# Kernel tuning notes

Hardware: AMD Instinct MI355X
Metric: run time of the kernel (lower is better)

## Reference

```python
import jax, jax.numpy as jnp
import numpy as np

B, Q, P = 8, 300, 5
RS, QS, CS, NC = 256, 768, 768, 396
HW = [64, 32, 16, 8]
POOL = [32, 16, 8, 4]
THR = 0.2


def _ln(x, g, b, eps=1e-5):
    m = x.mean(-1, keepdims=True)
    v = ((x - m) ** 2).mean(-1, keepdims=True)
    return (x - m) / jnp.sqrt(v + eps) * g + b


def _avgpool(x, oh, ow):
    # exact adaptive avg pool (output divides input)
    b, c, h, w = x.shape
    return x.reshape(b, c, oh, h // oh, ow, w // ow).mean((3, 5))


def setup_inputs() -> dict:
    key = jax.random.key(0)
    ks = jax.random.split(key, 40)
    inp = {}
    inp['pred_logits'] = jax.random.normal(ks[0], (B, Q, P), dtype=jnp.float32)
    inp['pred_boxes'] = jax.random.uniform(ks[1], (B, Q, 4), dtype=jnp.float32)
    inp['hs'] = jax.random.normal(ks[2], (B, Q, RS), dtype=jnp.float32)
    for s in range(4):
        inp[f'feat{s}'] = jax.random.normal(ks[3 + s], (B, 256, HW[s], HW[s]), dtype=jnp.float32)
        inp[f'pos{s}'] = jax.random.normal(ks[7 + s], (B, 256, HW[s], HW[s]), dtype=jnp.float32)
        inp[f'mask{s}'] = jax.random.bernoulli(ks[11 + s], 0.15, (B, HW[s], HW[s]))
        inp[f'convW{s}'] = jax.random.normal(ks[15 + s], (CS, 256), dtype=jnp.float32) * 0.02
        inp[f'convb{s}'] = jnp.zeros((CS,), jnp.float32)
        inp[f'lng{s}'] = jnp.ones((CS,), jnp.float32)
        inp[f'lnb{s}'] = jnp.zeros((CS,), jnp.float32)
    inp['learnable_query'] = jax.random.normal(ks[19], (P + 1, QS), dtype=jnp.float32)
    inp['Wq'] = jax.random.normal(ks[20], (RS, QS), dtype=jnp.float32) * 0.02
    inp['bq'] = jnp.zeros((QS,), jnp.float32)
    inp['qng'] = jnp.ones((QS,), jnp.float32)
    inp['qnb'] = jnp.zeros((QS,), jnp.float32)
    inp['W1'] = jax.random.normal(ks[21], (QS, QS), dtype=jnp.float32) * 0.02
    inp['b1'] = jnp.zeros((QS,), jnp.float32)
    inp['W2'] = jax.random.normal(ks[22], (QS, NC), dtype=jnp.float32) * 0.02
    inp['b2'] = jnp.zeros((NC,), jnp.float32)
    return inp


def _forward(pred_logits, pred_boxes, hs,
             feats, poss, masks, convWs, convbs, lngs, lnbs,
             learnable_query, Wq, bq, qng, qnb, W1, b1, W2, b2):
    del pred_boxes  # selected in the original but never used
    b = hs.shape[0]
    prob = jax.nn.sigmoid(pred_logits)                       # (B,Q,P)
    # per-prompt membership: logit_i > thr (implies max > thr)
    m = (prob > THR).astype(hs.dtype)                        # (B,Q,P)
    cnt = m.sum(1)                                           # (B,P)
    ssum = jnp.einsum('bqp,bqd->bpd', m, hs)                 # segment-sum over queries
    pooled = jnp.where(cnt[..., None] > 0,
                       ssum / jnp.maximum(cnt, 1.0)[..., None], 0.0)  # (B,P,RS)
    proj = pooled @ Wq + bq                                  # (B,P,QS)
    any_sel = jnp.any(prob.max(-1) > THR, axis=1)            # (B,)
    # if no query passed the global gate, prompt_hs is zeros WITHOUT projection
    prompt_hs = jnp.where(any_sel[:, None, None], proj, 0.0)
    prompt_query = learnable_query[1:] + prompt_hs           # (B,P,QS)
    cls_query = jnp.broadcast_to(learnable_query[0][None, None, :], (b, 1, QS))
    query_tokens = jnp.concatenate([cls_query, prompt_query], axis=1)
    query_tokens = _ln(query_tokens, qng, qnb)               # (B,P+1,QS)

    tokens = []
    for s in range(4):
        mask_f = masks[s][:, None, :, :].astype(feats[s].dtype)   # (B,1,H,W)
        x = (feats[s] + poss[s]) * (1.0 - mask_f)                 # masked_fill
        ctx = jnp.einsum('bchw,oc->bohw', x, convWs[s]) + convbs[s][None, :, None, None]
        p = _avgpool(ctx, POOL[s], POOL[s])
        mp = jnp.clip(_avgpool(1.0 - mask_f, POOL[s], POOL[s]), 1e-6, None)
        p = p / mp
        t = p.reshape(b, CS, -1).transpose(0, 2, 1)               # (B,T_s,CS)
        tokens.append(_ln(t, lngs[s], lnbs[s]))
    ctx_all = jnp.concatenate(tokens, axis=1)                     # (B,1360,CS)

    # encoder stand-in: fuse context into query tokens additively
    last = query_tokens + ctx_all.mean(1)[:, None, :]
    cls_logit = last[:, 0]
    prompt_logit = last[:, 1:].mean(1)
    h = jax.nn.relu((cls_logit + prompt_logit) @ W1 + b1)
    return h @ W2 + b2                                            # (B,NC)


def reference(pred_logits, pred_boxes, hs,
              feat0, pos0, mask0, convW0, convb0, lng0, lnb0,
              feat1, pos1, mask1, convW1, convb1, lng1, lnb1,
              feat2, pos2, mask2, convW2, convb2, lng2, lnb2,
              feat3, pos3, mask3, convW3, convb3, lng3, lnb3,
              learnable_query, Wq, bq, qng, qnb, W1, b1, W2, b2):
    return _forward(pred_logits, pred_boxes, hs,
                    [feat0, feat1, feat2, feat3],
                    [pos0, pos1, pos2, pos3],
                    [mask0, mask1, mask2, mask3],
                    [convW0, convW1, convW2, convW3],
                    [convb0, convb1, convb2, convb3],
                    [lng0, lng1, lng2, lng3],
                    [lnb0, lnb1, lnb2, lnb3],
                    learnable_query, Wq, bq, qng, qnb, W1, b1, W2, b2)
```

## Files before the change

### kernel.cpp

```cpp
#include <hip/hip_runtime.h>
#include <hip/hip_bf16.h>

#define Bn 8
#define Qn 300
#define Pn 5
#define RSn 256
#define QSn 768
#define NCn 396
#define MTOT 10880
#define THRL -1.3862943611198906f

typedef __attribute__((ext_vector_type(8))) short short8;
typedef __attribute__((ext_vector_type(4))) float float4v;

__device__ inline float wred(float v){
  #pragma unroll
  for (int off = 32; off; off >>= 1) v += __shfl_xor(v, off);
  return v;
}

__device__ __forceinline__ unsigned short f2bf(float f){
  union { float f; unsigned int u; } c; c.f = f;
  return (unsigned short)((c.u + 0x7FFF + ((c.u >> 16) & 1)) >> 16);
}

__device__ __forceinline__ void gld_lds16(const short* g, short* l){
  __builtin_amdgcn_global_load_lds(
      (const __attribute__((address_space(1))) void*)g,
      (__attribute__((address_space(3))) void*)l, 16, 0, 0);
}

__device__ __forceinline__ void mask_w(const void* M, int mbase, int mode, int i00, int H,
                                       float* w){
  if (mode == 0){
    int4 ma = *(const int4*)((const int*)M + mbase + i00);
    int4 mb = *(const int4*)((const int*)M + mbase + i00 + H);
    w[0]=ma.x?0.f:1.f; w[1]=ma.y?0.f:1.f; w[2]=ma.z?0.f:1.f; w[3]=ma.w?0.f:1.f;
    w[4]=mb.x?0.f:1.f; w[5]=mb.y?0.f:1.f; w[6]=mb.z?0.f:1.f; w[7]=mb.w?0.f:1.f;
  } else if (mode == 1){
    const unsigned char* Mb = (const unsigned char*)M + mbase;
    uchar4 ma = *(const uchar4*)(Mb + i00);
    uchar4 mb = *(const uchar4*)(Mb + i00 + H);
    w[0]=ma.x?0.f:1.f; w[1]=ma.y?0.f:1.f; w[2]=ma.z?0.f:1.f; w[3]=ma.w?0.f:1.f;
    w[4]=mb.x?0.f:1.f; w[5]=mb.y?0.f:1.f; w[6]=mb.z?0.f:1.f; w[7]=mb.w?0.f:1.f;
  } else {
    float4 ma = *(const float4*)((const float*)M + mbase + i00);
    float4 mb = *(const float4*)((const float*)M + mbase + i00 + H);
    w[0]=1.f-ma.x; w[1]=1.f-ma.y; w[2]=1.f-ma.z; w[3]=1.f-ma.w;
    w[4]=1.f-mb.x; w[5]=1.f-mb.y; w[6]=1.f-mb.z; w[7]=1.f-mb.w;
  }
}

__global__ __launch_bounds__(256, 4) void k_front(
    const float* cw0, const float* cw1, const float* cw2, const float* cw3,
    short* Wswz, const int* __restrict__ m0, int* det,
    const float* __restrict__ pl, const float* __restrict__ hs,
    float* pooled, int* flags, float* ctxsum, float* outz){
  int bx = blockIdx.x;
  int t = threadIdx.x;
  if (bx < 768){
    int s = bx / 192;
    int linear = (bx % 192)*256 + t;
    int q = linear & 63, n = linear >> 6;
    const float* src = (s==0)?cw0:(s==1)?cw1:(s==2)?cw2:cw3;
    float4 f = *(const float4*)(src + (size_t)n*256 + q*4);
    int kc = q >> 3, lk = (q >> 1) & 3, e0 = (q & 1)*4;
    short* dst = Wswz + ((size_t)(s*8 + kc))*24576 + lk*6144 + n*8 + e0;
    short4 sv;
    sv.x = (short)f2bf(f.x); sv.y = (short)f2bf(f.y);
    sv.z = (short)f2bf(f.z); sv.w = (short)f2bf(f.w);
    *(short4*)dst = sv;
    return;
  }
  if (bx == 768){
    __shared__ int r0[4], r1[4];
    const int* mm = m0 + t*32;
    int d0 = 0, d1 = 0;
    #pragma unroll 8
    for (int i = 0; i < 32; ++i){
      int v = mm[i];
      d0 |= (v != 0 && v != 1);
      d1 |= (v != 0 && v != 0x3F800000);
    }
    unsigned long long bal0 = __ballot(d0), bal1 = __ballot(d1);
    int wid = t >> 6;
    if ((t & 63) == 0){ r0[wid] = (bal0 != 0ull); r1[wid] = (bal1 != 0ull); }
    __syncthreads();
    if (t == 0){
      det[0] = r0[0] | r0[1] | r0[2] | r0[3];
      det[1] = r1[0] | r1[1] | r1[2] | r1[3];
    }
    return;
  }
  if (bx >= 821){
    int idx = ((bx - 821)*256 + t)*4;
    if (idx < Bn*NCn) *(float4*)(outz + idx) = (float4){0.f,0.f,0.f,0.f};
    return;
  }
  if (bx >= 809){
    int idx = ((bx - 809)*256 + t)*4;
    *(float4*)(ctxsum + idx) = (float4){0.f,0.f,0.f,0.f};
    return;
  }
  __shared__ float msk[Qn];
  int bb = (bx - 769) / Pn, p = (bx - 769) % Pn;
  for (int q = t; q < Qn; q += 256)
    msk[q] = (pl[(bb*Qn + q)*Pn + p] > THRL) ? 1.f : 0.f;
  __syncthreads();
  const float* hb = hs + (size_t)bb*Qn*RSn + t;
  float s0 = 0.f, s1 = 0.f, s2 = 0.f, s3 = 0.f, cnt = 0.f;
  for (int q = 0; q < Qn; q += 4){
    float m0v = msk[q], m1 = msk[q+1], m2 = msk[q+2], m3 = msk[q+3];
    cnt += m0v + m1 + m2 + m3;
    s0 = fmaf(m0v, hb[(size_t)(q  )*RSn], s0);
    s1 = fmaf(m1,  hb[(size_t)(q+1)*RSn], s1);
    s2 = fmaf(m2,  hb[(size_t)(q+2)*RSn], s2);
    s3 = fmaf(m3,  hb[(size_t)(q+3)*RSn], s3);
  }
  float ssum = (s0 + s1) + (s2 + s3);
  pooled[(bb*Pn + p)*RSn + t] = (cnt > 0.f) ? ssum / cnt : 0.f;
  if (t == 0) flags[bb*Pn + p] = (cnt > 0.f) ? 1 : 0;
}

__global__ __launch_bounds__(256, 4) void k_mid(
    const float* f0, const float* p0, const void* m0,
    const float* f1, const float* p1, const void* m1,
    const float* f2, const float* p2, const void* m2,
    const float* f3, const float* p3, const void* m3,
    const int* __restrict__ det, unsigned short* ATb, float* invmp,
    const float* __restrict__ lq, const float* __restrict__ Wq,
    const float* __restrict__ bq, const float* __restrict__ qng,
    const float* __restrict__ qnb, const float* __restrict__ pooled,
    const int* __restrict__ flags, float* qt){
  __shared__ float pq[256];
  __shared__ float s1s[4], s2s[4];
  int bx = blockIdx.x;
  int t = threadIdx.x;
  if (bx >= 48){
    int p = bx - 48;
    int mode = (det[0] == 0) ? 0 : ((det[1] == 0) ? 2 : 1);
    if (p < 1024){
      int b = p >> 7, r = p & 127;
      int c0 = (r >> 1)*4, half = r & 1;
      const int H = 64, HH = 4096;
      int tk = half*256 + t;
      int ph = tk >> 4, pw = tk & 15;
      int i00 = ph*128 + pw*4;
      int mbase = b*HH;
      float w[8];
      mask_w(m0, mbase, mode, i00, H, w);
      size_t plane = (size_t)(b*256 + c0)*HH + i00;
      const float* Fb = f0 + plane;
      const float* Pb = p0 + plane;
      float4 FA0 = *(const float4*)(Fb);
      float4 FB0 = *(const float4*)(Fb + H);
      float4 PA0 = *(const float4*)(Pb);
      float4 PB0 = *(const float4*)(Pb + H);
      float4 FA1 = *(const float4*)(Fb + HH);
      float4 FB1 = *(const float4*)(Fb + HH + H);
      float4 PA1 = *(const float4*)(Pb + HH);
      float4 PB1 = *(const float4*)(Pb + HH + H);
      float4 FA2 = *(const float4*)(Fb + 2*HH);
      float4 FB2 = *(const float4*)(Fb + 2*HH + H);
      float4 PA2 = *(const float4*)(Pb + 2*HH);
      float4 PB2 = *(const float4*)(Pb + 2*HH + H);
      float4 FA3 = *(const float4*)(Fb + 3*HH);
      float4 FB3 = *(const float4*)(Fb + 3*HH + H);
      float4 PA3 = *(const float4*)(Pb + 3*HH);
      float4 PB3 = *(const float4*)(Pb + 3*HH + H);
      float ms0 = w[0]+w[1]+w[4]+w[5];
      float ms1 = w[2]+w[3]+w[6]+w[7];
      float im0 = 1.f / fmaxf(ms0*0.25f, 1e-6f);
      float im1 = 1.f / fmaxf(ms1*0.25f, 1e-6f);
      float sc0 = 0.25f*im0, sc1 = 0.25f*im1;
      int mIdx = b*1024 + tk*2;
      #define DO_CH(cc, FA, FB, PA, PB) { \
        float x0 = (FA.x+PA.x)*w[0] + (FA.y+PA.y)*w[1] + (FB.x+PB.x)*w[4] + (FB.y+PB.y)*w[5]; \
        float x1 = (FA.z+PA.z)*w[2] + (FA.w+PA.w)*w[3] + (FB.z+PB.z)*w[6] + (FB.w+PB.w)*w[7]; \
        *(unsigned int*)(ATb + (size_t)(c0+cc)*MTOT + mIdx) = \
            (unsigned int)f2bf(x0*sc0) | ((unsigned int)f2bf(x1*sc1) << 16); }
      DO_CH(0, FA0, FB0, PA0, PB0)
      DO_CH(1, FA1, FB1, PA1, PB1)
      DO_CH(2, FA2, FB2, PA2, PB2)
      DO_CH(3, FA3, FB3, PA3, PB3)
      #undef DO_CH
      if (c0 == 0){ invmp[mIdx] = im0; invmp[mIdx+1] = im1; }
      return;
    }
    const float* F; const float* Pp; const void* M; int H, SB, T;
    int b, ch, tk; bool wr;
    if (p < 1536){
      int idx = p - 1024; b = idx >> 6;
      int c0 = (idx & 63)*4;
      F=f1; Pp=p1; M=m1; H=32; SB=8192; T=256;
      int ci = t >> 7; tk = t & 127;
      ch = c0 + ci*2; wr = (ch == 0);
      int ph = tk >> 3, pw = tk & 7;
      int i00 = ph*64 + pw*4;
      int HH = H*H, mbase = b*HH;
      float w[8]; mask_w(M, mbase, mode, i00, H, w);
      float ms0 = w[0]+w[1]+w[4]+w[5];
      float ms1 = w[2]+w[3]+w[6]+w[7];
      float im0 = 1.f / fmaxf(ms0*0.25f, 1e-6f);
      float im1 = 1.f / fmaxf(ms1*0.25f, 1e-6f);
      float sc0 = 0.25f*im0, sc1 = 0.25f*im1;
      int mIdx = SB + b*T + tk*2;
      size_t plane = (size_t)(b*256 + ch)*HH + i00;
      const float* Fb = F + plane; const float* Pb = Pp + plane;
      float4 FA0 = *(const float4*)(Fb);
      float4 FB0 = *(const float4*)(Fb + H);
      float4 PA0 = *(const float4*)(Pb);
      float4 PB0 = *(const float4*)(Pb + H);
      float4 FA1 = *(const float4*)(Fb + HH);
      float4 FB1 = *(const float4*)(Fb + HH + H);
      float4 PA1 = *(const float4*)(Pb + HH);
      float4 PB1 = *(const float4*)(Pb + HH + H);
      {
        float x0 = (FA0.x+PA0.x)*w[0] + (FA0.y+PA0.y)*w[1] + (FB0.x+PB0.x)*w[4] + (FB0.y+PB0.y)*w[5];
        float x1 = (FA0.z+PA0.z)*w[2] + (FA0.w+PA0.w)*w[3] + (FB0.z+PB0.z)*w[6] + (FB0.w+PB0.w)*w[7];
        *(unsigned int*)(ATb + (size_t)ch*MTOT + mIdx) =
            (unsigned int)f2bf(x0*sc0) | ((unsigned int)f2bf(x1*sc1) << 16);
        float y0 = (FA1.x+PA1.x)*w[0] + (FA1.y+PA1.y)*w[1] + (FB1.x+PB1.x)*w[4] + (FB1.y+PB1.y)*w[5];
        float y1 = (FA1.z+PA1.z)*w[2] + (FA1.w+PA1.w)*w[3] + (FB1.z+PB1.z)*w[6] + (FB1.w+PB1.w)*w[7];
        *(unsigned int*)(ATb + (size_t)(ch+1)*MTOT + mIdx) =
            (unsigned int)f2bf(y0*sc0) | ((unsigned int)f2bf(y1*sc1) << 16);
      }
      if (wr){ invmp[mIdx] = im0; invmp[mIdx+1] = im1; }
      return;
    }
    if (p < 1792){
      int idx = p - 1536; b = idx >> 5;
      ch = ((idx & 31)*8) + (t >> 5); tk = t & 31;
      F=f2; Pp=p2; M=m2; H=16; SB=10240; T=64;
    } else {
      int idx = p - 1792; b = idx >> 3;
      ch = ((idx & 7)*32) + (t >> 3); tk = t & 7;
      F=f3; Pp=p3; M=m3; H=8; SB=10752; T=16;
    }
    wr = (ch == 0);
    int OW2 = H >> 2;
    int ph = tk / OW2, pw = tk - ph*OW2;
    int i00 = ph*2*H + pw*4;
    int HH = H*H, mbase = b*HH;
    float w[8]; mask_w(M, mbase, mode, i00, H, w);
    float ms0 = w[0]+w[1]+w[4]+w[5];
    float ms1 = w[2]+w[3]+w[6]+w[7];
    float im0 = 1.f / fmaxf(ms0*0.25f, 1e-6f);
    float im1 = 1.f / fmaxf(ms1*0.25f, 1e-6f);
    float sc0 = 0.25f*im0, sc1 = 0.25f*im1;
    int mIdx = SB + b*T + tk*2;
    size_t plane = (size_t)(b*256 + ch)*HH + i00;
    const float* Fb = F + plane; const float* Pb = Pp + plane;
    float4 FA = *(const float4*)(Fb);
    float4 FB = *(const float4*)(Fb + H);
    float4 PA = *(const float4*)(Pb);
    float4 PB = *(const float4*)(Pb + H);
    float x0 = (FA.x+PA.x)*w[0] + (FA.y+PA.y)*w[1] + (FB.x+PB.x)*w[4] + (FB.y+PB.y)*w[5];
    float x1 = (FA.z+PA.z)*w[2] + (FA.w+PA.w)*w[3] + (FB.z+PB.z)*w[6] + (FB.w+PB.w)*w[7];
    *(unsigned int*)(ATb + (size_t)ch*MTOT + mIdx) =
        (unsigned int)f2bf(x0*sc0) | ((unsigned int)f2bf(x1*sc1) << 16);
    if (wr){ invmp[mIdx] = im0; invmp[mIdx+1] = im1; }
    return;
  }
  int b = bx / 6, j = bx % 6;
  float v0 = lq[j*QSn + t], v1 = lq[j*QSn + t + 256], v2 = lq[j*QSn + t + 512];
  int any = flags[b*Pn] | flags[b*Pn+1] | flags[b*Pn+2] | flags[b*Pn+3] | flags[b*Pn+4];
  if (j > 0 && any){
    pq[t] = pooled[(b*Pn + (j-1))*RSn + t];
    __syncthreads();
    float a0 = 0.f, a1 = 0.f, a2 = 0.f;
    #pragma unroll 8
    for (int c = 0; c < RSn; ++c){
      float pv = pq[c];
      a0 = fmaf(pv, Wq[c*QSn + t      ], a0);
      a1 = fmaf(pv, Wq[c*QSn + t + 256], a1);
      a2 = fmaf(pv, Wq[c*QSn + t + 512], a2);
    }
    v0 += a0 + bq[t]; v1 += a1 + bq[t+256]; v2 += a2 + bq[t+512];
  }
  float sm = v0 + v1 + v2, sq = v0*v0 + v1*v1 + v2*v2;
  sm = wred(sm); sq = wred(sq);
  int wid = t >> 6, lane = t & 63;
  if (lane == 0){ s1s[wid] = sm; s2s[wid] = sq; }
  __syncthreads();
  float S  = s1s[0] + s1s[1] + s1s[2] + s1s[3];
  float SQ = s2s[0] + s2s[1] + s2s[2] + s2s[3];
  float mu = S * (1.f/QSn), var = SQ * (1.f/QSn) - mu*mu;
  float rs = rsqrtf(var + 1e-5f);
  float* o = qt + (b*6 + j)*QSn;
  o[t      ] = (v0 - mu)*rs*qng[t      ] + qnb[t      ];
  o[t + 256] = (v1 - mu)*rs*qng[t + 256] + qnb[t + 256];
  o[t + 512] = (v2 - mu)*rs*qng[t + 512] + qnb[t + 512];
}

__global__ __launch_bounds__(256, 2) void k_gemm_ln(
    const unsigned short* __restrict__ ATb, const short* __restrict__ Wswz,
    const float* __restrict__ invmp,
    const float* cb0, const float* cb1, const float* cb2, const float* cb3,
    const float* lg0, const float* lb0, const float* lg1, const float* lb1,
    const float* lg2, const float* lb2, const float* lg3, const float* lb3,
    float* __restrict__ ctxsum){
  __shared__ short Bsh[24576];
  __shared__ float lsum[4][32], lsq[4][32];
  int m0 = blockIdx.x * 32;
  int s;
  if (m0 < 8192) s = 0;
  else if (m0 < 10240) s = 1;
  else if (m0 < 10752) s = 2;
  else s = 3;
  int b0, b1;
  if (s == 0){ b0 = m0 >> 10; b1 = b0; }
  else if (s == 1){ b0 = (m0 - 8192) >> 8; b1 = b0; }
  else if (s == 2){ b0 = (m0 - 10240) >> 6; b1 = b0; }
  else { b0 = (m0 - 10752) >> 4; b1 = b0 + 1; }
  const float *CB, *LG, *LB;
  if (s==0){ CB=cb0; LG=lg0; LB=lb0; }
  else if (s==1){ CB=cb1; LG=lg1; LB=lb1; }
  else if (s==2){ CB=cb2; LG=lg2; LB=lb2; }
  else { CB=cb3; LG=lg3; LB=lb3; }

  int t = threadIdx.x;
  int wid = t >> 6, l = t & 63;
  int lm = l & 15, lk = l >> 4;
  int nfb = wid * 12;

  {
    const unsigned short* src = ATb + (size_t)t*MTOT + m0;
    short8 a0 = *(const short8*)(src);
    short8 a1 = *(const short8*)(src + 8);
    short8 a2 = *(const short8*)(src + 16);
    short8 a3 = *(const short8*)(src + 24);
    #pragma unroll
    for (int e = 0; e < 8; ++e){
      Bsh[e*264 + t]      = a0[e];
      Bsh[(e+8)*264 + t]  = a1[e];
      Bsh[(e+16)*264 + t] = a2[e];
      Bsh[(e+24)*264 + t] = a3[e];
    }
  }
  __syncthreads();
  short8 aReg[2][8];
  #pragma unroll
  for (int mt = 0; mt < 2; ++mt)
    #pragma unroll
    for (int kc = 0; kc < 8; ++kc)
      aReg[mt][kc] = *(const short8*)(Bsh + (mt*16 + lm)*264 + kc*32 + lk*8);
  __syncthreads();

  float4v acc[2][12];
  #pragma unroll
  for (int mt = 0; mt < 2; ++mt)
    #pragma unroll
    for (int nf = 0; nf < 12; ++nf) acc[mt][nf] = (float4v){0.f,0.f,0.f,0.f};

  #pragma unroll
  for (int kc = 0; kc < 8; ++kc){
    const short* slice = Wswz + ((size_t)(s*8 + kc))*24576;
    #pragma unroll
    for (int j = 0; j < 12; ++j){
      int chunk = wid*12 + j;
      gld_lds16(slice + chunk*512 + l*8, Bsh + chunk*512);
    }
    __syncthreads();
    const short* bb = Bsh + lk*6144 + lm*8;
    #pragma unroll
    for (int nf = 0; nf < 12; ++nf){
      short8 bf = *(const short8*)(bb + (size_t)(nfb+nf)*128);
      acc[0][nf] = __builtin_amdgcn_mfma_f32_16x16x32_bf16(aReg[0][kc], bf, acc[0][nf], 0, 0, 0);
      acc[1][nf] = __builtin_amdgcn_mfma_f32_16x16x32_bf16(aReg[1][kc], bf, acc[1][nf], 0, 0, 0);
    }
    __syncthreads();
  }

  float im[2][4];
  #pragma unroll
  for (int mt = 0; mt < 2; ++mt)
    #pragma unroll
    for (int r = 0; r < 4; ++r) im[mt][r] = invmp[m0 + mt*16 + lk*4 + r];

  float sum[2][4] = {{0,0,0,0},{0,0,0,0}}, sq[2][4] = {{0,0,0,0},{0,0,0,0}};
  #pragma unroll
  for (int nf = 0; nf < 12; ++nf){
    float cbv = CB[(nfb+nf)*16 + lm];
    #pragma unroll
    for (int mt = 0; mt < 2; ++mt)
      #pragma unroll
      for (int r = 0; r < 4; ++r){
        float p = acc[mt][nf][r] + cbv*im[mt][r];
        acc[mt][nf][r] = p;
        sum[mt][r] += p;
        sq[mt][r] = fmaf(p, p, sq[mt][r]);
      }
  }
  #pragma unroll
  for (int mt = 0; mt < 2; ++mt)
    #pragma unroll
    for (int r = 0; r < 4; ++r){
      #pragma unroll
      for (int off = 1; off < 16; off <<= 1){
        sum[mt][r] += __shfl_xor(sum[mt][r], off);
        sq[mt][r]  += __shfl_xor(sq[mt][r],  off);
      }
    }
  if (lm == 0){
    #pragma unroll
    for (int mt = 0; mt < 2; ++mt)
      #pragma unroll
      for (int r = 0; r < 4; ++r){
        lsum[wid][mt*16 + lk*4 + r] = sum[mt][r];
        lsq[wid][mt*16 + lk*4 + r]  = sq[mt][r];
      }
  }
  __syncthreads();
  float mu[2][4], rs[2][4];
  #pragma unroll
  for (int mt = 0; mt < 2; ++mt)
    #pragma unroll
    for (int r = 0; r < 4; ++r){
      int row = mt*16 + lk*4 + r;
      float S  = lsum[0][row] + lsum[1][row] + lsum[2][row] + lsum[3][row];
      float SQ = lsq[0][row]  + lsq[1][row]  + lsq[2][row]  + lsq[3][row];
      mu[mt][r] = S * (1.f/768.f);
      float var = SQ * (1.f/768.f) - mu[mt][r]*mu[mt][r];
      rs[mt][r] = rsqrtf(var + 1e-5f);
    }
  #pragma unroll
  for (int nf = 0; nf < 12; ++nf){
    int n = (nfb+nf)*16 + lm;
    float g = LG[n], bb2 = LB[n];
    float tv0 = 0.f, tv1 = 0.f;
    #pragma unroll
    for (int r = 0; r < 4; ++r){
      tv0 += (acc[0][nf][r] - mu[0][r]) * rs[0][r];
      tv1 += (acc[1][nf][r] - mu[1][r]) * rs[1][r];
    }
    tv0 = tv0*g + 4.f*bb2;
    tv1 = tv1*g + 4.f*bb2;
    tv0 += __shfl_xor(tv0, 16); tv0 += __shfl_xor(tv0, 32);
    tv1 += __shfl_xor(tv1, 16); tv1 += __shfl_xor(tv1, 32);
    if (lk == 0){
      atomicAdd(&ctxsum[b0*768 + n], tv0);
      atomicAdd(&ctxsum[b1*768 + n], tv1);
    }
  }
}

__global__ void k_hpre(const float* __restrict__ qt, const float* __restrict__ ctxsum,
                       const float* __restrict__ W1, const float* __restrict__ b1,
                       float* __restrict__ hpre){
  __shared__ float vsh[Bn][192];
  int nc = blockIdx.x % 24, kc = blockIdx.x / 24;
  int n0 = nc*32, c0 = kc*192;
  int t = threadIdx.x;
  for (int i = t; i < Bn*192; i += 256){
    int b = i / 192, cl = i - b*192;
    int c = c0 + cl;
    const float* q = qt + (size_t)b*6*768;
    float pm = q[768+c] + q[2*768+c] + q[3*768+c] + q[4*768+c] + q[5*768+c];
    vsh[b][cl] = q[c] + 0.2f*pm + ctxsum[b*768 + c]*(1.f/680.f);
  }
  __syncthreads();
  int ow = t & 31, bi = t >> 5;
  int o = n0 + ow;
  float acc = 0.f;
  const float* w = W1 + (size_t)c0*768 + o;
  #pragma unroll 4
  for (int cl = 0; cl < 192; ++cl)
    acc = fmaf(vsh[bi][cl], w[(size_t)cl*768], acc);
  if (kc == 0) acc += b1[o];
  atomicAdd(&hpre[bi*768 + o], acc);
}

__global__ void k_out(const float* __restrict__ hpre, const float* __restrict__ W2,
                      const float* __restrict__ b2, float* __restrict__ out){
  __shared__ float hsh[Bn][192];
  int nc = blockIdx.x % 13, kc = blockIdx.x / 13;
  int n0 = nc*32, c0 = kc*192;
  int t = threadIdx.x;
  for (int i = t; i < Bn*192; i += 256){
    int b = i / 192, cl = i - b*192;
    hsh[b][cl] = fmaxf(hpre[b*768 + c0 + cl], 0.f);
  }
  __syncthreads();
  int ow = t & 31, bi = t >> 5;
  int o = n0 + ow;
  if (o >= NCn) return;
  float acc = 0.f;
  const float* w = W2 + (size_t)c0*NCn + o;
  #pragma unroll 4
  for (int cl = 0; cl < 192; ++cl)
    acc = fmaf(hsh[bi][cl], w[(size_t)cl*NCn], acc);
  if (kc == 0) acc += b2[o];
  atomicAdd(&out[bi*NCn + o], acc);
}

extern "C" void kernel_launch(void* const* d_in, const int* in_sizes, int n_in,
                              void* d_out, int out_size, void* d_ws, size_t ws_size,
                              hipStream_t stream){
  const float* pl = (const float*)d_in[0];
  const float* hs = (const float*)d_in[2];
  const float* feat[4]; const float* pos[4]; const void* mask[4];
  const float* cw[4]; const float* cb[4]; const float* lg[4]; const float* lb[4];
  for (int s = 0; s < 4; ++s){
    int base = 3 + 7*s;
    feat[s] = (const float*)d_in[base];
    pos[s]  = (const float*)d_in[base+1];
    mask[s] = d_in[base+2];
    cw[s]   = (const float*)d_in[base+3];
    cb[s]   = (const float*)d_in[base+4];
    lg[s]   = (const float*)d_in[base+5];
    lb[s]   = (const float*)d_in[base+6];
  }
  const float* lq  = (const float*)d_in[31];
  const float* Wq  = (const float*)d_in[32];
  const float* bq  = (const float*)d_in[33];
  const float* qng = (const float*)d_in[34];
  const float* qnb = (const float*)d_in[35];
  const float* W1  = (const float*)d_in[36];
  const float* b1  = (const float*)d_in[37];
  const float* W2  = (const float*)d_in[38];
  const float* b2  = (const float*)d_in[39];
  float* out = (float*)d_out;

  unsigned short* ATb = (unsigned short*)d_ws;
  short* Wswz   = (short*)(ATb + (size_t)256*MTOT);
  float* invmp  = (float*)(Wswz + (size_t)4*8*4*768*8);
  float* pooled = invmp + MTOT;
  float* qt     = pooled + 40*RSn;
  float* ctxsum = qt + Bn*6*QSn;
  float* hpre   = ctxsum + Bn*QSn;
  int*   det    = (int*)(hpre + Bn*QSn);
  int*   flags  = det + 4;

  k_front<<<825, 256, 0, stream>>>(cw[0], cw[1], cw[2], cw[3], Wswz,
                                   (const int*)mask[0], det, pl, hs, pooled, flags,
                                   ctxsum, out);
  k_mid<<<1904, 256, 0, stream>>>(feat[0], pos[0], mask[0],
                                  feat[1], pos[1], mask[1],
                                  feat[2], pos[2], mask[2],
                                  feat[3], pos[3], mask[3],
                                  det, ATb, invmp,
                                  lq, Wq, bq, qng, qnb, pooled, flags, qt);
  k_gemm_ln<<<340, 256, 0, stream>>>(ATb, Wswz, invmp,
                                     cb[0], cb[1], cb[2], cb[3],
                                     lg[0], lb[0], lg[1], lb[1],
                                     lg[2], lb[2], lg[3], lb[3], ctxsum);
  k_hpre<<<96, 256, 0, stream>>>(qt, ctxsum, W1, b1, hpre);
  k_out<<<52, 256, 0, stream>>>(hpre, W2, b2, out);
}
```

Baseline: 285.6 us.

## Fuse masked pooling into GEMM+LayerNorm kernel, drop bf16 activation buffer

Merges the pooling kernel into the GEMM+LN kernel. Each 32-row tile now computes its masked average pool directly from feat+pos into shared memory, so the bf16 activation buffer and inverse-mask array no longer go through global memory. This removes one launch and the global round trip of the pooled activations. In exchange, each block issues narrower float2 loads with less parallelism in the gather, and the query-norm blocks now share the heavier kernel's shared-memory footprint and occupancy.

```diff
diff --git a/kernel.cpp b/kernel.cpp
--- a/kernel.cpp
+++ b/kernel.cpp
@@ -30,30 +30,9 @@
       (__attribute__((address_space(3))) void*)l, 16, 0, 0);
 }
 
-__device__ __forceinline__ void mask_w(const void* M, int mbase, int mode, int i00, int H,
-                                       float* w){
-  if (mode == 0){
-    int4 ma = *(const int4*)((const int*)M + mbase + i00);
-    int4 mb = *(const int4*)((const int*)M + mbase + i00 + H);
-    w[0]=ma.x?0.f:1.f; w[1]=ma.y?0.f:1.f; w[2]=ma.z?0.f:1.f; w[3]=ma.w?0.f:1.f;
-    w[4]=mb.x?0.f:1.f; w[5]=mb.y?0.f:1.f; w[6]=mb.z?0.f:1.f; w[7]=mb.w?0.f:1.f;
-  } else if (mode == 1){
-    const unsigned char* Mb = (const unsigned char*)M + mbase;
-    uchar4 ma = *(const uchar4*)(Mb + i00);
-    uchar4 mb = *(const uchar4*)(Mb + i00 + H);
-    w[0]=ma.x?0.f:1.f; w[1]=ma.y?0.f:1.f; w[2]=ma.z?0.f:1.f; w[3]=ma.w?0.f:1.f;
-    w[4]=mb.x?0.f:1.f; w[5]=mb.y?0.f:1.f; w[6]=mb.z?0.f:1.f; w[7]=mb.w?0.f:1.f;
-  } else {
-    float4 ma = *(const float4*)((const float*)M + mbase + i00);
-    float4 mb = *(const float4*)((const float*)M + mbase + i00 + H);
-    w[0]=1.f-ma.x; w[1]=1.f-ma.y; w[2]=1.f-ma.z; w[3]=1.f-ma.w;
-    w[4]=1.f-mb.x; w[5]=1.f-mb.y; w[6]=1.f-mb.z; w[7]=1.f-mb.w;
-  }
-}
-
 __global__ __launch_bounds__(256, 4) void k_front(
     const float* cw0, const float* cw1, const float* cw2, const float* cw3,
-    short* Wswz, const int* __restrict__ m0, int* det,
+    short* Wswz, const int* __restrict__ mk0, int* det,
     const float* __restrict__ pl, const float* __restrict__ hs,
     float* pooled, int* flags, float* ctxsum, float* outz){
   int bx = blockIdx.x;
@@ -74,7 +53,7 @@
   }
   if (bx == 768){
     __shared__ int r0[4], r1[4];
-    const int* mm = m0 + t*32;
+    const int* mm = mk0 + t*32;
     int d0 = 0, d1 = 0;
     #pragma unroll 8
     for (int i = 0; i < 32; ++i){
@@ -122,230 +101,150 @@
   if (t == 0) flags[bb*Pn + p] = (cnt > 0.f) ? 1 : 0;
 }
 
-__global__ __launch_bounds__(256, 4) void k_mid(
-    const float* f0, const float* p0, const void* m0,
-    const float* f1, const float* p1, const void* m1,
-    const float* f2, const float* p2, const void* m2,
-    const float* f3, const float* p3, const void* m3,
-    const int* __restrict__ det, unsigned short* ATb, float* invmp,
+__global__ __launch_bounds__(256, 2) void k_pgemm(
+    const float* fe0, const float* po0, const void* ma0,
+    const float* fe1, const float* po1, const void* ma1,
+    const float* fe2, const float* po2, const void* ma2,
+    const float* fe3, const float* po3, const void* ma3,
+    const int* __restrict__ det, const short* __restrict__ Wswz,
+    const float* cb0, const float* cb1, const float* cb2, const float* cb3,
+    const float* lg0, const float* lb0, const float* lg1, const float* lb1,
+    const float* lg2, const float* lb2, const float* lg3, const float* lb3,
+    float* __restrict__ ctxsum,
     const float* __restrict__ lq, const float* __restrict__ Wq,
     const float* __restrict__ bq, const float* __restrict__ qng,
     const float* __restrict__ qnb, const float* __restrict__ pooled,
     const int* __restrict__ flags, float* qt){
+  __shared__ short Bsh[24576];
+  __shared__ short As[32*264];
+  __shared__ float wls[32][4];
+  __shared__ float scls[32], imls[32];
+  __shared__ float lsum[4][32], lsq[4][32];
   __shared__ float pq[256];
   __shared__ float s1s[4], s2s[4];
-  int bx = blockIdx.x;
+  int blk = blockIdx.x;
   int t = threadIdx.x;
-  if (bx >= 48){
-    int p = bx - 48;
-    int mode = (det[0] == 0) ? 0 : ((det[1] == 0) ? 2 : 1);
-    if (p < 1024){
-      int b = p >> 7, r = p & 127;
-      int c0 = (r >> 1)*4, half = r & 1;
-      const int H = 64, HH = 4096;
-      int tk = half*256 + t;
-      int ph = tk >> 4, pw = tk & 15;
-      int i00 = ph*128 + pw*4;
-      int mbase = b*HH;
-      float w[8];
-      mask_w(m0, mbase, mode, i00, H, w);
-      size_t plane = (size_t)(b*256 + c0)*HH + i00;
-      const float* Fb = f0 + plane;
-      const float* Pb = p0 + plane;
-      float4 FA0 = *(const float4*)(Fb);
-      float4 FB0 = *(const float4*)(Fb + H);
-      float4 PA0 = *(const float4*)(Pb);
-      float4 PB0 = *(const float4*)(Pb + H);
-      float4 FA1 = *(const float4*)(Fb + HH);
-      float4 FB1 = *(const float4*)(Fb + HH + H);
-      float4 PA1 = *(const float4*)(Pb + HH);
-      float4 PB1 = *(const float4*)(Pb + HH + H);
-      float4 FA2 = *(const float4*)(Fb + 2*HH);
-      float4 FB2 = *(const float4*)(Fb + 2*HH + H);
-      float4 PA2 = *(const float4*)(Pb + 2*HH);
-      float4 PB2 = *(const float4*)(Pb + 2*HH + H);
-      float4 FA3 = *(const float4*)(Fb + 3*HH);
-      float4 FB3 = *(const float4*)(Fb + 3*HH + H);
-      float4 PA3 = *(const float4*)(Pb + 3*HH);
-      float4 PB3 = *(const float4*)(Pb + 3*HH + H);
-      float ms0 = w[0]+w[1]+w[4]+w[5];
-      float ms1 = w[2]+w[3]+w[6]+w[7];
-      float im0 = 1.f / fmaxf(ms0*0.25f, 1e-6f);
-      float im1 = 1.f / fmaxf(ms1*0.25f, 1e-6f);
-      float sc0 = 0.25f*im0, sc1 = 0.25f*im1;
-      int mIdx = b*1024 + tk*2;
-      #define DO_CH(cc, FA, FB, PA, PB) { \
-        float x0 = (FA.x+PA.x)*w[0] + (FA.y+PA.y)*w[1] + (FB.x+PB.x)*w[4] + (FB.y+PB.y)*w[5]; \
-        float x1 = (FA.z+PA.z)*w[2] + (FA.w+PA.w)*w[3] + (FB.z+PB.z)*w[6] + (FB.w+PB.w)*w[7]; \
-        *(unsigned int*)(ATb + (size_t)(c0+cc)*MTOT + mIdx) = \
-            (unsigned int)f2bf(x0*sc0) | ((unsigned int)f2bf(x1*sc1) << 16); }
-      DO_CH(0, FA0, FB0, PA0, PB0)
-      DO_CH(1, FA1, FB1, PA1, PB1)
-      DO_CH(2, FA2, FB2, PA2, PB2)
-      DO_CH(3, FA3, FB3, PA3, PB3)
-      #undef DO_CH
-      if (c0 == 0){ invmp[mIdx] = im0; invmp[mIdx+1] = im1; }
-      return;
-    }
-    const float* F; const float* Pp; const void* M; int H, SB, T;
-    int b, ch, tk; bool wr;
-    if (p < 1536){
-      int idx = p - 1024; b = idx >> 6;
-      int c0 = (idx & 63)*4;
-      F=f1; Pp=p1; M=m1; H=32; SB=8192; T=256;
-      int ci = t >> 7; tk = t & 127;
-      ch = c0 + ci*2; wr = (ch == 0);
-      int ph = tk >> 3, pw = tk & 7;
-      int i00 = ph*64 + pw*4;
-      int HH = H*H, mbase = b*HH;
-      float w[8]; mask_w(M, mbase, mode, i00, H, w);
-      float ms0 = w[0]+w[1]+w[4]+w[5];
-      float ms1 = w[2]+w[3]+w[6]+w[7];
-      float im0 = 1.f / fmaxf(ms0*0.25f, 1e-6f);
-      float im1 = 1.f / fmaxf(ms1*0.25f, 1e-6f);
-      float sc0 = 0.25f*im0, sc1 = 0.25f*im1;
-      int mIdx = SB + b*T + tk*2;
-      size_t plane = (size_t)(b*256 + ch)*HH + i00;
-      const float* Fb = F + plane; const float* Pb = Pp + plane;
-      float4 FA0 = *(const float4*)(Fb);
-      float4 FB0 = *(const float4*)(Fb + H);
-      float4 PA0 = *(const float4*)(Pb);
-      float4 PB0 = *(const float4*)(Pb + H);
-      float4 FA1 = *(const float4*)(Fb + HH);
-      float4 FB1 = *(const float4*)(Fb + HH + H);
-      float4 PA1 = *(const float4*)(Pb + HH);
-      float4 PB1 = *(const float4*)(Pb + HH + H);
-      {
-        float x0 = (FA0.x+PA0.x)*w[0] + (FA0.y+PA0.y)*w[1] + (FB0.x+PB0.x)*w[4] + (FB0.y+PB0.y)*w[5];
-        float x1 = (FA0.z+PA0.z)*w[2] + (FA0.w+PA0.w)*w[3] + (FB0.z+PB0.z)*w[6] + (FB0.w+PB0.w)*w[7];
-        *(unsigned int*)(ATb + (size_t)ch*MTOT + mIdx) =
-            (unsigned int)f2bf(x0*sc0) | ((unsigned int)f2bf(x1*sc1) << 16);
-        float y0 = (FA1.x+PA1.x)*w[0] + (FA1.y+PA1.y)*w[1] + (FB1.x+PB1.x)*w[4] + (FB1.y+PB1.y)*w[5];
-        float y1 = (FA1.z+PA1.z)*w[2] + (FA1.w+PA1.w)*w[3] + (FB1.z+PB1.z)*w[6] + (FB1.w+PB1.w)*w[7];
-        *(unsigned int*)(ATb + (size_t)(ch+1)*MTOT + mIdx) =
-            (unsigned int)f2bf(y0*sc0) | ((unsigned int)f2bf(y1*sc1) << 16);
+
+  if (blk >= 340){
+    int qbx = blk - 340;
+    int b = qbx / 6, j = qbx % 6;
+    float v0 = lq[j*QSn + t], v1 = lq[j*QSn + t + 256], v2 = lq[j*QSn + t + 512];
+    int any = flags[b*Pn] | flags[b*Pn+1] | flags[b*Pn+2] | flags[b*Pn+3] | flags[b*Pn+4];
+    if (j > 0 && any){
+      pq[t] = pooled[(b*Pn + (j-1))*RSn + t];
+      __syncthreads();
+      float a0 = 0.f, a1 = 0.f, a2 = 0.f;
+      #pragma unroll 8
+      for (int c = 0; c < RSn; ++c){
+        float pv = pq[c];
+        a0 = fmaf(pv, Wq[c*QSn + t      ], a0);
+        a1 = fmaf(pv, Wq[c*QSn + t + 256], a1);
+        a2 = fmaf(pv, Wq[c*QSn + t + 512], a2);
       }
-      if (wr){ invmp[mIdx] = im0; invmp[mIdx+1] = im1; }
-      return;
-    }
-    if (p < 1792){
-      int idx = p - 1536; b = idx >> 5;
-      ch = ((idx & 31)*8) + (t >> 5); tk = t & 31;
-      F=f2; Pp=p2; M=m2; H=16; SB=10240; T=64;
+      v0 += a0 + bq[t]; v1 += a1 + bq[t+256]; v2 += a2 + bq[t+512];
+    }
+    float sm = v0 + v1 + v2, sq = v0*v0 + v1*v1 + v2*v2;
+    sm = wred(sm); sq = wred(sq);
+    int wid = t >> 6, lane = t & 63;
+    if (lane == 0){ s1s[wid] = sm; s2s[wid] = sq; }
+    __syncthreads();
+    float S  = s1s[0] + s1s[1] + s1s[2] + s1s[3];
+    float SQ = s2s[0] + s2s[1] + s2s[2] + s2s[3];
+    float mu = S * (1.f/QSn), var = SQ * (1.f/QSn) - mu*mu;
+    float rs = rsqrtf(var + 1e-5f);
+    float* o = qt + (b*6 + j)*QSn;
+    o[t      ] = (v0 - mu)*rs*qng[t      ] + qnb[t      ];
+    o[t + 256] = (v1 - mu)*rs*qng[t + 256] + qnb[t + 256];
+    o[t + 512] = (v2 - mu)*rs*qng[t + 512] + qnb[t + 512];
+    return;
+  }
+
+  int m0 = blk * 32;
+  int s, H, OWlog, b0, b1;
+  const float *F, *Pp; const void* M;
+  const float *CB, *LG, *LB;
+  if (m0 < 8192){ s=0; F=fe0; Pp=po0; M=ma0; H=64; OWlog=5; b0=m0>>10; b1=b0;
+                  CB=cb0; LG=lg0; LB=lb0; }
+  else if (m0 < 10240){ s=1; F=fe1; Pp=po1; M=ma1; H=32; OWlog=4; b0=(m0-8192)>>8; b1=b0;
+                  CB=cb1; LG=lg1; LB=lb1; }
+  else if (m0 < 10752){ s=2; F=fe2; Pp=po2; M=ma2; H=16; OWlog=3; b0=(m0-10240)>>6; b1=b0;
+                  CB=cb2; LG=lg2; LB=lb2; }
+  else { s=3; F=fe3; Pp=po3; M=ma3; H=8; OWlog=2; b0=(m0-10752)>>4; b1=b0+1;
+                  CB=cb3; LG=lg3; LB=lb3; }
+  int HH = H*H;
+  int OWm = (H >> 1) - 1;
+  int mode = (det[0] == 0) ? 0 : ((det[1] == 0) ? 2 : 1);
+
+  int slot = t & 31;
+  int gm = m0 + slot;
+  int bb, ltl;
+  if (s == 0){ bb = gm >> 10; ltl = gm & 1023; }
+  else if (s == 1){ bb = (gm - 8192) >> 8; ltl = gm & 255; }
+  else if (s == 2){ bb = (gm - 10240) >> 6; ltl = gm & 63; }
+  else { bb = (gm - 10752) >> 4; ltl = gm & 15; }
+  int ph = ltl >> OWlog, pw = ltl & OWm;
+  int i00 = ph*2*H + pw*2;
+  int mbase = bb*HH;
+
+  if (t < 32){
+    float w0, w1, w2, w3;
+    if (mode == 0){
+      const int* Mi = (const int*)M + mbase + i00;
+      int2 ma = *(const int2*)(Mi);
+      int2 mb = *(const int2*)(Mi + H);
+      w0 = ma.x?0.f:1.f; w1 = ma.y?0.f:1.f; w2 = mb.x?0.f:1.f; w3 = mb.y?0.f:1.f;
+    } else if (mode == 1){
+      const unsigned char* Mb = (const unsigned char*)M + mbase + i00;
+      w0 = Mb[0]?0.f:1.f; w1 = Mb[1]?0.f:1.f; w2 = Mb[H]?0.f:1.f; w3 = Mb[H+1]?0.f:1.f;
     } else {
-      int idx = p - 1792; b = idx >> 3;
-      ch = ((idx & 7)*32) + (t >> 3); tk = t & 7;
-      F=f3; Pp=p3; M=m3; H=8; SB=10752; T=16;
-    }
-    wr = (ch == 0);
-    int OW2 = H >> 2;
-    int ph = tk / OW2, pw = tk - ph*OW2;
-    int i00 = ph*2*H + pw*4;
-    int HH = H*H, mbase = b*HH;
-    float w[8]; mask_w(M, mbase, mode, i00, H, w);
-    float ms0 = w[0]+w[1]+w[4]+w[5];
-    float ms1 = w[2]+w[3]+w[6]+w[7];
-    float im0 = 1.f / fmaxf(ms0*0.25f, 1e-6f);
-    float im1 = 1.f / fmaxf(ms1*0.25f, 1e-6f);
-    float sc0 = 0.25f*im0, sc1 = 0.25f*im1;
-    int mIdx = SB + b*T + tk*2;
-    size_t plane = (size_t)(b*256 + ch)*HH + i00;
-    const float* Fb = F + plane; const float* Pb = Pp + plane;
-    float4 FA = *(const float4*)(Fb);
-    float4 FB = *(const float4*)(Fb + H);
-    float4 PA = *(const float4*)(Pb);
-    float4 PB = *(const float4*)(Pb + H);
-    float x0 = (FA.x+PA.x)*w[0] + (FA.y+PA.y)*w[1] + (FB.x+PB.x)*w[4] + (FB.y+PB.y)*w[5];
-    float x1 = (FA.z+PA.z)*w[2] + (FA.w+PA.w)*w[3] + (FB.z+PB.z)*w[6] + (FB.w+PB.w)*w[7];
-    *(unsigned int*)(ATb + (size_t)ch*MTOT + mIdx) =
-        (unsigned int)f2bf(x0*sc0) | ((unsigned int)f2bf(x1*sc1) << 16);
-    if (wr){ invmp[mIdx] = im0; invmp[mIdx+1] = im1; }
-    return;
-  }
-  int b = bx / 6, j = bx % 6;
-  float v0 = lq[j*QSn + t], v1 = lq[j*QSn + t + 256], v2 = lq[j*QSn + t + 512];
-  int any = flags[b*Pn] | flags[b*Pn+1] | flags[b*Pn+2] | flags[b*Pn+3] | flags[b*Pn+4];
-  if (j > 0 && any){
-    pq[t] = pooled[(b*Pn + (j-1))*RSn + t];
-    __syncthreads();
-    float a0 = 0.f, a1 = 0.f, a2 = 0.f;
-    #pragma unroll 8
-    for (int c = 0; c < RSn; ++c){
-      float pv = pq[c];
-      a0 = fmaf(pv, Wq[c*QSn + t      ], a0);
-      a1 = fmaf(pv, Wq[c*QSn + t + 256], a1);
-      a2 = fmaf(pv, Wq[c*QSn + t + 512], a2);
-    }
-    v0 += a0 + bq[t]; v1 += a1 + bq[t+256]; v2 += a2 + bq[t+512];
-  }
-  float sm = v0 + v1 + v2, sq = v0*v0 + v1*v1 + v2*v2;
-  sm = wred(sm); sq = wred(sq);
-  int wid = t >> 6, lane = t & 63;
-  if (lane == 0){ s1s[wid] = sm; s2s[wid] = sq; }
-  __syncthreads();
-  float S  = s1s[0] + s1s[1] + s1s[2] + s1s[3];
-  float SQ = s2s[0] + s2s[1] + s2s[2] + s2s[3];
-  float mu = S * (1.f/QSn), var = SQ * (1.f/QSn) - mu*mu;
-  float rs = rsqrtf(var + 1e-5f);
-  float* o = qt + (b*6 + j)*QSn;
-  o[t      ] = (v0 - mu)*rs*qng[t      ] + qnb[t      ];
-  o[t + 256] = (v1 - mu)*rs*qng[t + 256] + qnb[t + 256];
-  o[t + 512] = (v2 - mu)*rs*qng[t + 512] + qnb[t + 512];
-}
-
-__global__ __launch_bounds__(256, 2) void k_gemm_ln(
-    const unsigned short* __restrict__ ATb, const short* __restrict__ Wswz,
-    const float* __restrict__ invmp,
-    const float* cb0, const float* cb1, const float* cb2, const float* cb3,
-    const float* lg0, const float* lb0, const float* lg1, const float* lb1,
-    const float* lg2, const float* lb2, const float* lg3, const float* lb3,
-    float* __restrict__ ctxsum){
-  __shared__ short Bsh[24576];
-  __shared__ float lsum[4][32], lsq[4][32];
-  int m0 = blockIdx.x * 32;
-  int s;
-  if (m0 < 8192) s = 0;
-  else if (m0 < 10240) s = 1;
-  else if (m0 < 10752) s = 2;
-  else s = 3;
-  int b0, b1;
-  if (s == 0){ b0 = m0 >> 10; b1 = b0; }
-  else if (s == 1){ b0 = (m0 - 8192) >> 8; b1 = b0; }
-  else if (s == 2){ b0 = (m0 - 10240) >> 6; b1 = b0; }
-  else { b0 = (m0 - 10752) >> 4; b1 = b0 + 1; }
-  const float *CB, *LG, *LB;
-  if (s==0){ CB=cb0; LG=lg0; LB=lb0; }
-  else if (s==1){ CB=cb1; LG=lg1; LB=lb1; }
-  else if (s==2){ CB=cb2; LG=lg2; LB=lb2; }
-  else { CB=cb3; LG=lg3; LB=lb3; }
-
-  int t = threadIdx.x;
+      const float* Mf = (const float*)M + mbase + i00;
+      float2 ma = *(const float2*)(Mf);
+      float2 mb = *(const float2*)(Mf + H);
+      w0 = 1.f-ma.x; w1 = 1.f-ma.y; w2 = 1.f-mb.x; w3 = 1.f-mb.y;
+    }
+    float msum = w0 + w1 + w2 + w3;
+    float im = 1.f / fmaxf(msum*0.25f, 1e-6f);
+    wls[t][0] = w0; wls[t][1] = w1; wls[t][2] = w2; wls[t][3] = w3;
+    scls[t] = 0.25f*im; imls[t] = im;
+  }
+  __syncthreads();
+
+  {
+    float w0 = wls[slot][0], w1 = wls[slot][1], w2 = wls[slot][2], w3 = wls[slot][3];
+    float sc = scls[slot];
+    int chb = (t >> 5) * 2;
+    size_t base = (size_t)(bb*256 + chb)*HH + i00;
+    const float* Fp = F + base;
+    const float* Pq = Pp + base;
+    const int stride = 16*HH;
+    #pragma unroll 2
+    for (int r = 0; r < 16; ++r){
+      float2 fa0 = *(const float2*)(Fp);
+      float2 fb0 = *(const float2*)(Fp + H);
+      float2 pa0 = *(const float2*)(Pq);
+      float2 pb0 = *(const float2*)(Pq + H);
+      float2 fa1 = *(const float2*)(Fp + HH);
+      float2 fb1 = *(const float2*)(Fp + HH + H);
+      float2 pa1 = *(const float2*)(Pq + HH);
+      float2 pb1 = *(const float2*)(Pq + HH + H);
+      float x0 = (fa0.x+pa0.x)*w0 + (fa0.y+pa0.y)*w1 + (fb0.x+pb0.x)*w2 + (fb0.y+pb0.y)*w3;
+      float x1 = (fa1.x+pa1.x)*w0 + (fa1.y+pa1.y)*w1 + (fb1.x+pb1.x)*w2 + (fb1.y+pb1.y)*w3;
+      *(unsigned int*)(&As[slot*264 + chb + r*16]) =
+          (unsigned int)f2bf(x0*sc) | ((unsigned int)f2bf(x1*sc) << 16);
+      Fp += stride; Pq += stride;
+    }
+  }
+  __syncthreads();
+
   int wid = t >> 6, l = t & 63;
   int lm = l & 15, lk = l >> 4;
   int nfb = wid * 12;
-
-  {
-    const unsigned short* src = ATb + (size_t)t*MTOT + m0;
-    short8 a0 = *(const short8*)(src);
-    short8 a1 = *(const short8*)(src + 8);
-    short8 a2 = *(const short8*)(src + 16);
-    short8 a3 = *(const short8*)(src + 24);
-    #pragma unroll
-    for (int e = 0; e < 8; ++e){
-      Bsh[e*264 + t]      = a0[e];
-      Bsh[(e+8)*264 + t]  = a1[e];
-      Bsh[(e+16)*264 + t] = a2[e];
-      Bsh[(e+24)*264 + t] = a3[e];
-    }
-  }
-  __syncthreads();
   short8 aReg[2][8];
   #pragma unroll
   for (int mt = 0; mt < 2; ++mt)
     #pragma unroll
     for (int kc = 0; kc < 8; ++kc)
-      aReg[mt][kc] = *(const short8*)(Bsh + (mt*16 + lm)*264 + kc*32 + lk*8);
-  __syncthreads();
+      aReg[mt][kc] = *(const short8*)(As + (mt*16 + lm)*264 + kc*32 + lk*8);
 
   float4v acc[2][12];
   #pragma unroll
@@ -362,10 +261,10 @@
       gld_lds16(slice + chunk*512 + l*8, Bsh + chunk*512);
     }
     __syncthreads();
-    const short* bb = Bsh + lk*6144 + lm*8;
+    const short* bb2 = Bsh + lk*6144 + lm*8;
     #pragma unroll
     for (int nf = 0; nf < 12; ++nf){
-      short8 bf = *(const short8*)(bb + (size_t)(nfb+nf)*128);
+      short8 bf = *(const short8*)(bb2 + (size_t)(nfb+nf)*128);
       acc[0][nf] = __builtin_amdgcn_mfma_f32_16x16x32_bf16(aReg[0][kc], bf, acc[0][nf], 0, 0, 0);
       acc[1][nf] = __builtin_amdgcn_mfma_f32_16x16x32_bf16(aReg[1][kc], bf, acc[1][nf], 0, 0, 0);
     }
@@ -376,7 +275,7 @@
   #pragma unroll
   for (int mt = 0; mt < 2; ++mt)
     #pragma unroll
-    for (int r = 0; r < 4; ++r) im[mt][r] = invmp[m0 + mt*16 + lk*4 + r];
+    for (int r = 0; r < 4; ++r) im[mt][r] = imls[mt*16 + lk*4 + r];
 
   float sum[2][4] = {{0,0,0,0},{0,0,0,0}}, sq[2][4] = {{0,0,0,0},{0,0,0,0}};
   #pragma unroll
@@ -427,15 +326,15 @@
   #pragma unroll
   for (int nf = 0; nf < 12; ++nf){
     int n = (nfb+nf)*16 + lm;
-    float g = LG[n], bb2 = LB[n];
+    float g = LG[n], bv = LB[n];
     float tv0 = 0.f, tv1 = 0.f;
     #pragma unroll
     for (int r = 0; r < 4; ++r){
       tv0 += (acc[0][nf][r] - mu[0][r]) * rs[0][r];
       tv1 += (acc[1][nf][r] - mu[1][r]) * rs[1][r];
     }
-    tv0 = tv0*g + 4.f*bb2;
-    tv1 = tv1*g + 4.f*bb2;
+    tv0 = tv0*g + 4.f*bv;
+    tv1 = tv1*g + 4.f*bv;
     tv0 += __shfl_xor(tv0, 16); tv0 += __shfl_xor(tv0, 32);
     tv1 += __shfl_xor(tv1, 16); tv1 += __shfl_xor(tv1, 32);
     if (lk == 0){
@@ -522,10 +421,8 @@
   const float* b2  = (const float*)d_in[39];
   float* out = (float*)d_out;
 
-  unsigned short* ATb = (unsigned short*)d_ws;
-  short* Wswz   = (short*)(ATb + (size_t)256*MTOT);
-  float* invmp  = (float*)(Wswz + (size_t)4*8*4*768*8);
-  float* pooled = invmp + MTOT;
+  short* Wswz   = (short*)d_ws;
+  float* pooled = (float*)(Wswz + (size_t)4*8*4*768*8);
   float* qt     = pooled + 40*RSn;
   float* ctxsum = qt + Bn*6*QSn;
   float* hpre   = ctxsum + Bn*QSn;
@@ -535,16 +432,15 @@
   k_front<<<825, 256, 0, stream>>>(cw[0], cw[1], cw[2], cw[3], Wswz,
                                    (const int*)mask[0], det, pl, hs, pooled, flags,
                                    ctxsum, out);
-  k_mid<<<1904, 256, 0, stream>>>(feat[0], pos[0], mask[0],
-                                  feat[1], pos[1], mask[1],
-                                  feat[2], pos[2], mask[2],
-                                  feat[3], pos[3], mask[3],
-                                  det, ATb, invmp,
-                                  lq, Wq, bq, qng, qnb, pooled, flags, qt);
-  k_gemm_ln<<<340, 256, 0, stream>>>(ATb, Wswz, invmp,
-                                     cb[0], cb[1], cb[2], cb[3],
-                                     lg[0], lb[0], lg[1], lb[1],
-                                     lg[2], lb[2], lg[3], lb[3], ctxsum);
+  k_pgemm<<<388, 256, 0, stream>>>(feat[0], pos[0], mask[0],
+                                   feat[1], pos[1], mask[1],
+                                   feat[2], pos[2], mask[2],
+                                   feat[3], pos[3], mask[3],
+                                   det, Wswz,
+                                   cb[0], cb[1], cb[2], cb[3],
+                                   lg[0], lb[0], lg[1], lb[1],
+                                   lg[2], lb[2], lg[3], lb[3], ctxsum,
+                                   lq, Wq, bq, qng, qnb, pooled, flags, qt);
   k_hpre<<<96, 256, 0, stream>>>(qt, ctxsum, W1, b1, hpre);
   k_out<<<52, 256, 0, stream>>>(hpre, W2, b2, out);
 }
```

After: 272.9 us. 1.05x faster.
